# Performance work log

Measured on AMD Instinct MI355X. Metric: run time of the kernel, lower is better.

Reference implementation:

```python
import jax, jax.numpy as jnp
import numpy as np

BLOCK = 8
INDICES_RADIUS = 127.0  # radius of int8 index dtype


def _dct_matrix(n: int) -> np.ndarray:
    """Orthonormal DCT-II matrix M[element, frequency] matching transforms.cosine."""
    e = np.arange(n)[:, None].astype(np.float64)
    f = np.arange(n)[None, :].astype(np.float64)
    m = np.sqrt(2.0 / n) * np.cos(np.pi * (2.0 * e + 1.0) * f / (2.0 * n))
    m[:, 0] = np.sqrt(1.0 / n)
    return m.astype(np.float32)


def setup_inputs() -> dict:
    key = jax.random.key(0)
    x = jax.random.normal(key, (8192, 8192), dtype=jnp.float32)
    dct = jnp.asarray(_dct_matrix(BLOCK))
    return {"x": x, "dct": dct}


def reference(x, dct):
    # Block splitting: blocked[b1,b2,e1,e2] = x[8*b1+e1, 8*b2+e2]
    H, W = x.shape  # already multiples of BLOCK, so padding is a no-op
    b1, b2 = H // BLOCK, W // BLOCK
    blocked = x.reshape(b1, BLOCK, b2, BLOCK).transpose(0, 2, 1, 3)  # (b1,b2,8,8)
    # Separable blockwise DCT: contract intra-block axes with M[element,freq]
    coeffs = jnp.einsum("bcef,eg,fh->bcgh", blocked, dct, dct)
    # mask is all-ones 8x8 -> row-major flatten of intra-block coefficients
    flat = coeffs.reshape(b1, b2, BLOCK * BLOCK)  # (b1,b2,64)
    # bin(): per-block inf-norm then uniform quantization to int8 bins
    biggest = jnp.max(jnp.abs(flat), axis=-1)  # (b1,b2)
    indices = jnp.round(flat * (INDICES_RADIUS / biggest[..., None])).astype(jnp.int8)
    return indices, biggest
```

## Files before the change

### kernel.cpp

```cpp
#include <hip/hip_runtime.h>


#define IMG_H 8192
#define IMG_W 8192
#define NB1 (IMG_H / 8)
#define NB2 (IMG_W / 8)

__global__ __launch_bounds__(256, 4) void dct_quant_kernel(
    const float* __restrict__ x,
    float* __restrict__ out_idx,
    float* __restrict__ out_big)
{
    constexpr float c1 = 0.4903926402016152f;
    constexpr float c2 = 0.4619397662556434f;
    constexpr float c3 = 0.4157348061512726f;
    constexpr float c4 = 0.35355339059327373f;
    constexpr float c5 = 0.2777851165098011f;
    constexpr float c6 = 0.1913417161825449f;
    constexpr float c7 = 0.0975451610080642f;
    constexpr float M[8][8] = {
        { c4,  c1,  c2,  c3,  c4,  c5,  c6,  c7},
        { c4,  c3,  c6, -c7, -c4, -c1, -c2, -c5},
        { c4,  c5, -c6, -c1, -c4,  c7,  c2,  c3},
        { c4,  c7, -c2, -c5,  c4,  c3, -c6, -c1},
        { c4, -c7, -c2,  c5,  c4, -c3, -c6,  c1},
        { c4, -c5, -c6,  c1, -c4, -c7,  c2, -c3},
        { c4, -c3,  c6,  c7, -c4,  c1, -c2,  c5},
        { c4, -c1,  c2, -c3,  c4, -c5,  c6, -c7},
    };

    const int tid = blockIdx.x * blockDim.x + threadIdx.x;
    const int b1 = tid >> 10;
    const int b2 = tid & 1023;

    const float* src = x + (size_t)b1 * 8 * IMG_W + (size_t)b2 * 8;

    float B[8][8];
#pragma unroll
    for (int e = 0; e < 8; ++e) {
        const float4* p = (const float4*)(src + (size_t)e * IMG_W);
        float4 lo = p[0];
        float4 hi = p[1];
        B[e][0] = lo.x; B[e][1] = lo.y; B[e][2] = lo.z; B[e][3] = lo.w;
        B[e][4] = hi.x; B[e][5] = hi.y; B[e][6] = hi.z; B[e][7] = hi.w;
    }

#pragma unroll
    for (int e = 0; e < 8; ++e) {
        float t[8];
#pragma unroll
        for (int h = 0; h < 8; ++h) {
            float s = B[e][0] * M[0][h];
#pragma unroll
            for (int f = 1; f < 8; ++f) s = fmaf(B[e][f], M[f][h], s);
            t[h] = s;
        }
#pragma unroll
        for (int h = 0; h < 8; ++h) B[e][h] = t[h];
    }

    float big = 0.0f;
#pragma unroll
    for (int h = 0; h < 8; ++h) {
        float t[8];
#pragma unroll
        for (int g = 0; g < 8; ++g) {
            float s = M[0][g] * B[0][h];
#pragma unroll
            for (int e = 1; e < 8; ++e) s = fmaf(M[e][g], B[e][h], s);
            t[g] = s;
        }
#pragma unroll
        for (int g = 0; g < 8; ++g) {
            B[g][h] = t[g];
            big = fmaxf(big, fabsf(t[g]));
        }
    }

    const float scale = 127.0f / big;
    float* o = out_idx + (size_t)tid * 64;
#pragma unroll
    for (int g = 0; g < 8; ++g) {
        float4 v0, v1;
        v0.x = rintf(B[g][0] * scale);
        v0.y = rintf(B[g][1] * scale);
        v0.z = rintf(B[g][2] * scale);
        v0.w = rintf(B[g][3] * scale);
        v1.x = rintf(B[g][4] * scale);
        v1.y = rintf(B[g][5] * scale);
        v1.z = rintf(B[g][6] * scale);
        v1.w = rintf(B[g][7] * scale);
        ((float4*)o)[2 * g]     = v0;
        ((float4*)o)[2 * g + 1] = v1;
    }
    out_big[tid] = big;
}

extern "C" void kernel_launch(void* const* d_in, const int* in_sizes, int n_in,
                              void* d_out, int out_size, void* d_ws, size_t ws_size,
                              hipStream_t stream) {
    const float* x = (const float*)d_in[0];
    float* out = (float*)d_out;
    float* out_idx = out;
    float* out_big = out + (size_t)NB1 * NB2 * 64;

    const int nthreads = NB1 * NB2;
    dct_quant_kernel<<<nthreads / 256, 256, 0, stream>>>(x, out_idx, out_big);
}
```

Measured before the change: 470.1 us.

## Split DCT passes across threads via shared-memory 64x64 tiles

Each workgroup now processes a 64x64 tile. Threads compute the row DCT in registers and stage the results in padded LDS, then the column DCT is computed by 8 threads per block. Those threads combine the per-block max with cross-lane shuffles and write outputs with per-lane scalar stores. The aim is more threads per block of work and lower register pressure, at the cost of a barrier, LDS traffic and narrower global stores.

```diff
diff --git a/kernel.cpp b/kernel.cpp
--- a/kernel.cpp
+++ b/kernel.cpp
@@ -5,95 +5,118 @@
 #define IMG_W 8192
 #define NB1 (IMG_H / 8)
 #define NB2 (IMG_W / 8)
+#define LSTR 68
 
 __global__ __launch_bounds__(256, 4) void dct_quant_kernel(
     const float* __restrict__ x,
     float* __restrict__ out_idx,
     float* __restrict__ out_big)
 {
-    constexpr float c1 = 0.4903926402016152f;
-    constexpr float c2 = 0.4619397662556434f;
-    constexpr float c3 = 0.4157348061512726f;
-    constexpr float c4 = 0.35355339059327373f;
-    constexpr float c5 = 0.2777851165098011f;
-    constexpr float c6 = 0.1913417161825449f;
-    constexpr float c7 = 0.0975451610080642f;
+    constexpr float k1 = 0.4903926402016152f;
+    constexpr float k2 = 0.4619397662556434f;
+    constexpr float k3 = 0.4157348061512726f;
+    constexpr float k4 = 0.35355339059327373f;
+    constexpr float k5 = 0.2777851165098011f;
+    constexpr float k6 = 0.1913417161825449f;
+    constexpr float k7 = 0.0975451610080642f;
     constexpr float M[8][8] = {
-        { c4,  c1,  c2,  c3,  c4,  c5,  c6,  c7},
-        { c4,  c3,  c6, -c7, -c4, -c1, -c2, -c5},
-        { c4,  c5, -c6, -c1, -c4,  c7,  c2,  c3},
-        { c4,  c7, -c2, -c5,  c4,  c3, -c6, -c1},
-        { c4, -c7, -c2,  c5,  c4, -c3, -c6,  c1},
-        { c4, -c5, -c6,  c1, -c4, -c7,  c2, -c3},
-        { c4, -c3,  c6,  c7, -c4,  c1, -c2,  c5},
-        { c4, -c1,  c2, -c3,  c4, -c5,  c6, -c7},
+        { k4,  k1,  k2,  k3,  k4,  k5,  k6,  k7},
+        { k4,  k3,  k6, -k7, -k4, -k1, -k2, -k5},
+        { k4,  k5, -k6, -k1, -k4,  k7,  k2,  k3},
+        { k4,  k7, -k2, -k5,  k4,  k3, -k6, -k1},
+        { k4, -k7, -k2,  k5,  k4, -k3, -k6,  k1},
+        { k4, -k5, -k6,  k1, -k4, -k7,  k2, -k3},
+        { k4, -k3,  k6,  k7, -k4,  k1, -k2,  k5},
+        { k4, -k1,  k2, -k3,  k4, -k5,  k6, -k7},
     };
 
-    const int tid = blockIdx.x * blockDim.x + threadIdx.x;
-    const int b1 = tid >> 10;
-    const int b2 = tid & 1023;
+    __shared__ float t1[64 * LSTR];
 
-    const float* src = x + (size_t)b1 * 8 * IMG_W + (size_t)b2 * 8;
+    const int t   = threadIdx.x;
+    const int tb1 = blockIdx.x >> 7;
+    const int tb2 = blockIdx.x & 127;
 
-    float B[8][8];
+    const float* tile = x + (size_t)tb1 * 64 * IMG_W + (size_t)tb2 * 64;
+
+    {
+        const int r0 = t >> 3;
+        const int c0 = t & 7;
+
+        const float4* p0 = (const float4*)(tile + (size_t)r0 * IMG_W + c0 * 8);
+        const float4* p1 = (const float4*)(tile + (size_t)(r0 + 32) * IMG_W + c0 * 8);
+        const float4 a0 = p0[0];
+        const float4 a1 = p0[1];
+        const float4 b0 = p1[0];
+        const float4 b1 = p1[1];
+
+        {
+            const float u[8] = {a0.x, a0.y, a0.z, a0.w, a1.x, a1.y, a1.z, a1.w};
+            float w[8];
 #pragma unroll
-    for (int e = 0; e < 8; ++e) {
-        const float4* p = (const float4*)(src + (size_t)e * IMG_W);
-        float4 lo = p[0];
-        float4 hi = p[1];
-        B[e][0] = lo.x; B[e][1] = lo.y; B[e][2] = lo.z; B[e][3] = lo.w;
-        B[e][4] = hi.x; B[e][5] = hi.y; B[e][6] = hi.z; B[e][7] = hi.w;
+            for (int h = 0; h < 8; ++h) {
+                float s = u[0] * M[0][h];
+#pragma unroll
+                for (int f = 1; f < 8; ++f) s = fmaf(u[f], M[f][h], s);
+                w[h] = s;
+            }
+            float* d = &t1[r0 * LSTR + c0 * 8];
+            ((float4*)d)[0] = make_float4(w[0], w[1], w[2], w[3]);
+            ((float4*)d)[1] = make_float4(w[4], w[5], w[6], w[7]);
+        }
+        {
+            const float u[8] = {b0.x, b0.y, b0.z, b0.w, b1.x, b1.y, b1.z, b1.w};
+            float w[8];
+#pragma unroll
+            for (int h = 0; h < 8; ++h) {
+                float s = u[0] * M[0][h];
+#pragma unroll
+                for (int f = 1; f < 8; ++f) s = fmaf(u[f], M[f][h], s);
+                w[h] = s;
+            }
+            float* d = &t1[(r0 + 32) * LSTR + c0 * 8];
+            ((float4*)d)[0] = make_float4(w[0], w[1], w[2], w[3]);
+            ((float4*)d)[1] = make_float4(w[4], w[5], w[6], w[7]);
+        }
     }
+    __syncthreads();
 
 #pragma unroll
-    for (int e = 0; e < 8; ++e) {
-        float t[8];
+    for (int k = 0; k < 2; ++k) {
+        const int s   = t + k * 256;
+        const int bb  = s >> 3;
+        const int h   = s & 7;
+        const int bbr = bb >> 3;
+        const int bbc = bb & 7;
+
+        const float* col = &t1[bbr * 8 * LSTR + bbc * 8 + h];
+        float v[8];
 #pragma unroll
-        for (int h = 0; h < 8; ++h) {
-            float s = B[e][0] * M[0][h];
-#pragma unroll
-            for (int f = 1; f < 8; ++f) s = fmaf(B[e][f], M[f][h], s);
-            t[h] = s;
-        }
-#pragma unroll
-        for (int h = 0; h < 8; ++h) B[e][h] = t[h];
-    }
+        for (int e = 0; e < 8; ++e) v[e] = col[e * LSTR];
 
-    float big = 0.0f;
-#pragma unroll
-    for (int h = 0; h < 8; ++h) {
-        float t[8];
+        float c[8];
+        float big = 0.0f;
 #pragma unroll
         for (int g = 0; g < 8; ++g) {
-            float s = M[0][g] * B[0][h];
+            float s2 = M[0][g] * v[0];
 #pragma unroll
-            for (int e = 1; e < 8; ++e) s = fmaf(M[e][g], B[e][h], s);
-            t[g] = s;
+            for (int e = 1; e < 8; ++e) s2 = fmaf(M[e][g], v[e], s2);
+            c[g] = s2;
+            big = fmaxf(big, fabsf(s2));
         }
+        big = fmaxf(big, __shfl_xor(big, 1));
+        big = fmaxf(big, __shfl_xor(big, 2));
+        big = fmaxf(big, __shfl_xor(big, 4));
+
+        const float scale = 127.0f / big;
+        const int b1 = tb1 * 8 + bbr;
+        const int b2 = tb2 * 8 + bbc;
+        const size_t blk = (size_t)b1 * NB2 + b2;
+
+        float* o = out_idx + blk * 64 + h;
 #pragma unroll
-        for (int g = 0; g < 8; ++g) {
-            B[g][h] = t[g];
-            big = fmaxf(big, fabsf(t[g]));
-        }
+        for (int g = 0; g < 8; ++g) o[g * 8] = rintf(c[g] * scale);
+        if (h == 0) out_big[blk] = big;
     }
-
-    const float scale = 127.0f / big;
-    float* o = out_idx + (size_t)tid * 64;
-#pragma unroll
-    for (int g = 0; g < 8; ++g) {
-        float4 v0, v1;
-        v0.x = rintf(B[g][0] * scale);
-        v0.y = rintf(B[g][1] * scale);
-        v0.z = rintf(B[g][2] * scale);
-        v0.w = rintf(B[g][3] * scale);
-        v1.x = rintf(B[g][4] * scale);
-        v1.y = rintf(B[g][5] * scale);
-        v1.z = rintf(B[g][6] * scale);
-        v1.w = rintf(B[g][7] * scale);
-        ((float4*)o)[2 * g]     = v0;
-        ((float4*)o)[2 * g + 1] = v1;
-    }
-    out_big[tid] = big;
 }
 
 extern "C" void kernel_launch(void* const* d_in, const int* in_sizes, int n_in,
@@ -104,6 +127,5 @@
     float* out_idx = out;
     float* out_big = out + (size_t)NB1 * NB2 * 64;
 
-    const int nthreads = NB1 * NB2;
-    dct_quant_kernel<<<nthreads / 256, 256, 0, stream>>>(x, out_idx, out_big);
+    dct_quant_kernel<<<16384, 256, 0, stream>>>(x, out_idx, out_big);
 }
```

Result: faster. 442.9 us (-5.8%).
